# Optimization experiments

Hardware: AMD Instinct MI355X
Metric: run time of the kernel (lower is better)

Reference implementation:

```python
import jax, jax.numpy as jnp
import numpy as np

N = 500000
TOL = 0.01
ALPHA = 0.1
SLOPE = 0.01
EPS = 1e-10


def smooth_relu(x):
    # 0 for x<0; x^2/2 for 0<=x<1; x-1/2 for x>=1 (C1 smooth ReLU)
    return jnp.where(x < 0, 0.0, jnp.where(x < 1, 0.5 * x * x, x - 0.5))


def leaky_relu(x):
    return jnp.where(x >= 0, x, SLOPE * x)


def _xavier(key, shape):
    fan_out, fan_in = shape
    std = np.sqrt(2.0 / (fan_in + fan_out)).astype(np.float32)
    return jax.random.normal(key, shape, dtype=jnp.float32) * std


def setup_inputs() -> dict:
    key = jax.random.key(0)
    ks = jax.random.split(key, 16)
    inp = {
        'X': jax.random.normal(ks[0], (N, 2), dtype=jnp.float32),
        'Xstable': jnp.zeros((N, 2), dtype=jnp.float32),
        'Vl1_w': _xavier(ks[1], (64, 2)),
        'V2x_w': _xavier(ks[2], (64, 2)),
        'V2z_w': _xavier(ks[3], (64, 64)),
        'V3x_w': _xavier(ks[4], (64, 2)),
        'V3z_w': _xavier(ks[5], (64, 64)),
        'Vfx_w': _xavier(ks[6], (1, 2)),
        'Vfz_w': _xavier(ks[7], (1, 64)),
        'f1_w': _xavier(ks[8], (128, 2)),
        'f1_b': jnp.zeros((128,), dtype=jnp.float32),
        'f2_w': _xavier(ks[9], (128, 128)),
        'f2_b': jnp.zeros((128,), dtype=jnp.float32),
        'f3_w': _xavier(ks[10], (128, 128)),
        'f3_b': jnp.zeros((128,), dtype=jnp.float32),
        'f4_w': _xavier(ks[11], (128, 128)),
        'f4_b': jnp.zeros((128,), dtype=jnp.float32),
        'f5_w': _xavier(ks[12], (128, 128)),
        'f5_b': jnp.zeros((128,), dtype=jnp.float32),
        'ff_w': _xavier(ks[13], (2, 128)),
        'ff_b': jnp.zeros((2,), dtype=jnp.float32),
    }
    return inp


def _V_forward(X, Xstable, Vl1_w, V2x_w, V2z_w, V3x_w, V3z_w, Vfx_w, Vfz_w):
    d = X - Xstable                                  # [N,2]
    z1 = smooth_relu(d @ Vl1_w.T)                    # [N,64]
    z2 = smooth_relu(d @ V2x_w.T + z1 @ V2z_w.T)     # [N,64]
    z3 = smooth_relu(d @ V3x_w.T + z2 @ V3z_w.T)     # [N,64]
    zf = smooth_relu(d @ Vfx_w.T + z3 @ Vfz_w.T)     # [N,1]
    vsum = TOL * jnp.sum(d * d, axis=1, keepdims=True)
    return smooth_relu(zf) + vsum                    # [N,1]


def _fhat_forward(X, f1_w, f1_b, f2_w, f2_b, f3_w, f3_b, f4_w, f4_b, f5_w, f5_b, ff_w, ff_b):
    h = leaky_relu(X @ f1_w.T + f1_b)
    h = leaky_relu(h @ f2_w.T + f2_b)
    h = leaky_relu(h @ f3_w.T + f3_b)
    h = leaky_relu(h @ f4_w.T + f4_b)
    h = leaky_relu(h @ f5_w.T + f5_b)
    return h @ ff_w.T + ff_b                         # [N,2]


def reference(X, Xstable, Vl1_w, V2x_w, V2z_w, V3x_w, V3z_w, Vfx_w, Vfz_w,
              f1_w, f1_b, f2_w, f2_b, f3_w, f3_b, f4_w, f4_b, f5_w, f5_b, ff_w, ff_b):
    def Vfn(Xv):
        return _V_forward(Xv, Xstable, Vl1_w, V2x_w, V2z_w, V3x_w, V3z_w, Vfx_w, Vfz_w)

    V, pullback = jax.vjp(Vfn, X)
    gradV = pullback(jnp.ones_like(V))[0]            # dV/dX, [N,2]

    f_hat = _fhat_forward(X, f1_w, f1_b, f2_w, f2_b, f3_w, f3_b,
                          f4_w, f4_b, f5_w, f5_b, ff_w, ff_b)

    Vnorm = jnp.sum(gradV * gradV, axis=1, keepdims=True)      # [N,1]
    fh_V = jnp.sum(f_hat * gradV, axis=1, keepdims=True)       # [N,1]
    f_mul = jax.nn.relu(fh_V + ALPHA * V) / (Vnorm + EPS)      # [N,1]
    f = f_hat - gradV * f_mul                                  # [N,2]
    return f
```

## Files before the change

kernel.cpp:

```cpp
#include <hip/hip_runtime.h>


typedef _Float16 v2h __attribute__((ext_vector_type(2)));
typedef __fp16   v2hf __attribute__((ext_vector_type(2)));
typedef _Float16 v4h __attribute__((ext_vector_type(4)));
typedef _Float16 v8h __attribute__((ext_vector_type(8)));
typedef float    v4f __attribute__((ext_vector_type(4)));

__device__ __forceinline__ v2h cvt_pk(float a, float b){
  v2hf r = __builtin_amdgcn_cvt_pkrtz(a, b);
  union { v2hf f; v2h h; } u; u.f = r;
  return u.h;
}

#define NPTS 500000
#define FUSED_GRID ((NPTS + 255) / 256)

#define BAR_LDS() asm volatile("s_waitcnt lgkmcnt(0)\n\ts_barrier" ::: "memory")

#define OFF_FW    0
#define OFF_V2Z   65536
#define OFF_V3Z   69632
#define OFF_V2ZT  73728
#define OFF_V3ZT  77824
#define OFF_VL1T  81920
#define OFF_V2XT  82048
#define OFF_V3XT  82176
#define OFF_VFZ   82304
#define OFF_FFW   82368
#define OFF_F1W   82624
#define OFF_F1P   82880
#define W16_DATA  86976
#define W16_TOTAL (W16_DATA + 2048)

__device__ __align__(16) _Float16 g_w16[W16_TOTAL];

__device__ __forceinline__ float srelu(float x){
  float c = fminf(fmaxf(x, 0.f), 1.f);
  return c * fmaf(-0.5f, c, x);
}
__device__ __forceinline__ float sreluD(float x){
  return fminf(fmaxf(x, 0.f), 1.f);
}
__device__ __forceinline__ float sreluD_from_z(float z){
  return fminf(sqrtf(2.f * z), 1.f);
}

__device__ __forceinline__ v2h lrelu_pk(float a, float b){
  v2h x = cvt_pk(a, b);
  v2h m = x * (v2h){(_Float16)0.01f, (_Float16)0.01f};
  return __builtin_elementwise_max(x, m);
}
__device__ __forceinline__ v2h srelu_pk(float a, float b){
  v2h x = cvt_pk(a, b);
  const v2h z0 = (v2h){(_Float16)0.f, (_Float16)0.f};
  const v2h o1 = (v2h){(_Float16)1.f, (_Float16)1.f};
  const v2h hf = (v2h){(_Float16)0.5f, (_Float16)0.5f};
  v2h c = __builtin_elementwise_min(__builtin_elementwise_max(x, z0), o1);
  v2h t = x - c * hf;
  return c * t;
}

__global__ __launch_bounds__(256) void prep_kernel(
  const float* __restrict__ f2w, const float* __restrict__ f3w,
  const float* __restrict__ f4w, const float* __restrict__ f5w,
  const float* __restrict__ V2z, const float* __restrict__ V3z,
  const float* __restrict__ Vl1, const float* __restrict__ V2x,
  const float* __restrict__ V3x, const float* __restrict__ Vfz,
  const float* __restrict__ ffw, const float* __restrict__ f1w)
{
  const int i = blockIdx.x * 256 + threadIdx.x;
  if (i >= W16_TOTAL) return;
  if (i >= W16_DATA){ g_w16[i] = (_Float16)0.f; return; }
  float v;
  if (i < 65536){
    const float* W[4] = {f2w, f3w, f4w, f5w};
    v = W[i >> 14][i & 16383];
  } else if (i < 69632)  v = V2z[i - 65536];
  else if (i < 73728)    v = V3z[i - 69632];
  else if (i < 77824){ int r = i - 73728; v = V2z[(r & 63)*64 + (r >> 6)]; }
  else if (i < 81920){ int r = i - 77824; v = V3z[(r & 63)*64 + (r >> 6)]; }
  else if (i < 82048){ int r = i - 81920; v = Vl1[(r & 63)*2 + (r >> 6)]; }
  else if (i < 82176){ int r = i - 82048; v = V2x[(r & 63)*2 + (r >> 6)]; }
  else if (i < 82304){ int r = i - 82176; v = V3x[(r & 63)*2 + (r >> 6)]; }
  else if (i < 82368)    v = Vfz[i - 82304];
  else if (i < 82624)    v = ffw[i - 82368];
  else if (i < 82880)    v = f1w[i - 82624];
  else { int r = i - 82880; int k = r & 31; v = (k < 2) ? f1w[(r >> 5)*2 + k] : 0.f; }
  g_w16[i] = (_Float16)v;
}

__device__ __forceinline__ void fh_layer(_Float16* H,
    const _Float16* __restrict__ Wl, const float* __restrict__ Bp,
    int w, int lm, int q)
{
  const v4f bv = *(const v4f*)(Bp + w*16 + q*4);
  v4f acc[16];
#pragma unroll
  for (int nt = 0; nt < 16; ++nt) acc[nt] = bv;

#pragma unroll
  for (int kt = 0; kt < 4; ++kt){
    const int sw = ((kt*4 + q) ^ lm) << 3;
    v8h A = *(const v8h*)(Wl + (w*16 + lm)*128 + kt*32 + q*8);
#pragma unroll
    for (int nt = 0; nt < 16; ++nt){
      v8h B = *(const v8h*)(H + (nt*16 + lm)*128 + sw);
      acc[nt] = __builtin_amdgcn_mfma_f32_16x16x32_f16(A, B, acc[nt], 0,0,0);
    }
  }
  BAR_LDS();
  const int o0 = w*16 + q*4;
  const int coff = (((o0 >> 3) ^ lm) << 3) + (o0 & 7);
#pragma unroll
  for (int nt = 0; nt < 16; ++nt){
    v4h hv;
    *(v2h*)&hv       = lrelu_pk(acc[nt][0], acc[nt][1]);
    *((v2h*)&hv + 1) = lrelu_pk(acc[nt][2], acc[nt][3]);
    *(v4h*)(H + (nt*16 + lm)*128 + coff) = hv;
  }
  BAR_LDS();
}

__device__ __forceinline__ void vfwd2_l2(_Float16* zoutA, _Float16* zoutB,
    const _Float16* __restrict__ Wz,
    const _Float16* __restrict__ WxT,
    const _Float16* __restrict__ Wl1T,
    float dA0, float dA1, float dB0, float dB1, int lm, int q)
{
  v4f accA[4], accB[4];
#pragma unroll
  for (int mt = 0; mt < 4; ++mt){
    accA[mt] = (v4f){0.f,0.f,0.f,0.f};
    accB[mt] = (v4f){0.f,0.f,0.f,0.f};
  }
  const int rs = lm & 7;
#pragma unroll
  for (int kt = 0; kt < 2; ++kt){
    v8h w0 = *(const v8h*)(Wl1T + kt*32 + q*8);
    v8h w1 = *(const v8h*)(Wl1T + 64 + kt*32 + q*8);
    v8h BA, BB;
#pragma unroll
    for (int j2 = 0; j2 < 4; ++j2){
      const float a0 = (float)w0[2*j2  ], a1 = (float)w0[2*j2+1];
      const float c0 = (float)w1[2*j2  ], c1 = (float)w1[2*j2+1];
      ((v2h*)&BA)[j2] = srelu_pk(fmaf(dA0,a0,dA1*c0), fmaf(dA0,a1,dA1*c1));
      ((v2h*)&BB)[j2] = srelu_pk(fmaf(dB0,a0,dB1*c0), fmaf(dB0,a1,dB1*c1));
    }
#pragma unroll
    for (int mt = 0; mt < 4; ++mt){
      v8h A = *(const v8h*)(Wz + (mt*16 + lm)*64 + kt*32 + q*8);
      accA[mt] = __builtin_amdgcn_mfma_f32_16x16x32_f16(A, BA, accA[mt], 0,0,0);
      accB[mt] = __builtin_amdgcn_mfma_f32_16x16x32_f16(A, BB, accB[mt], 0,0,0);
    }
  }
#pragma unroll
  for (int mt = 0; mt < 4; ++mt){
    const int o0 = mt*16 + q*4;
    const int off = (((o0 >> 3) ^ rs) << 3) + (o0 & 7);
    float vA[4], vB[4];
#pragma unroll
    for (int reg = 0; reg < 4; ++reg){
      const float wx0 = (float)WxT[o0 + reg];
      const float wx1 = (float)WxT[64 + o0 + reg];
      vA[reg] = accA[mt][reg] + wx0*dA0 + wx1*dA1;
      vB[reg] = accB[mt][reg] + wx0*dB0 + wx1*dB1;
    }
    v4h hA, hB;
    *(v2h*)&hA       = srelu_pk(vA[0], vA[1]);
    *((v2h*)&hA + 1) = srelu_pk(vA[2], vA[3]);
    *(v2h*)&hB       = srelu_pk(vB[0], vB[1]);
    *((v2h*)&hB + 1) = srelu_pk(vB[2], vB[3]);
    *(v4h*)(zoutA + lm*64 + off) = hA;
    *(v4h*)(zoutB + lm*64 + off) = hB;
  }
}

__device__ __forceinline__ void vfwd2(const _Float16* zinA, _Float16* zoutA,
    const _Float16* zinB, _Float16* zoutB,
    const _Float16* __restrict__ Wz, const _Float16* __restrict__ WxT,
    float dA0, float dA1, float dB0, float dB1, int lm, int q)
{
  v4f accA[4], accB[4];
#pragma unroll
  for (int mt = 0; mt < 4; ++mt){
    accA[mt] = (v4f){0.f,0.f,0.f,0.f};
    accB[mt] = (v4f){0.f,0.f,0.f,0.f};
  }
  const int rs = lm & 7;
#pragma unroll
  for (int kt = 0; kt < 2; ++kt){
    const int sw = (((kt*4 + q) ^ rs) << 3);
    v8h BA = *(const v8h*)(zinA + lm*64 + sw);
    v8h BB = *(const v8h*)(zinB + lm*64 + sw);
#pragma unroll
    for (int mt = 0; mt < 4; ++mt){
      v8h A = *(const v8h*)(Wz + (mt*16 + lm)*64 + kt*32 + q*8);
      accA[mt] = __builtin_amdgcn_mfma_f32_16x16x32_f16(A, BA, accA[mt], 0,0,0);
      accB[mt] = __builtin_amdgcn_mfma_f32_16x16x32_f16(A, BB, accB[mt], 0,0,0);
    }
  }
#pragma unroll
  for (int mt = 0; mt < 4; ++mt){
    const int o0 = mt*16 + q*4;
    const int off = (((o0 >> 3) ^ rs) << 3) + (o0 & 7);
    float vA[4], vB[4];
#pragma unroll
    for (int reg = 0; reg < 4; ++reg){
      const float wx0 = (float)WxT[o0 + reg];
      const float wx1 = (float)WxT[64 + o0 + reg];
      vA[reg] = accA[mt][reg] + wx0*dA0 + wx1*dA1;
      vB[reg] = accB[mt][reg] + wx0*dB0 + wx1*dB1;
    }
    v4h hA, hB;
    *(v2h*)&hA       = srelu_pk(vA[0], vA[1]);
    *((v2h*)&hA + 1) = srelu_pk(vA[2], vA[3]);
    *(v2h*)&hB       = srelu_pk(vB[0], vB[1]);
    *((v2h*)&hB + 1) = srelu_pk(vB[2], vB[3]);
    *(v4h*)(zoutA + lm*64 + off) = hA;
    *(v4h*)(zoutB + lm*64 + off) = hB;
  }
}

__device__ __forceinline__ void vbwd2(const _Float16* ginA, _Float16* zioA,
    const _Float16* ginB, _Float16* zioB,
    const _Float16* __restrict__ WT, int lm, int q)
{
  v4f accA[4], accB[4];
#pragma unroll
  for (int mt = 0; mt < 4; ++mt){
    accA[mt] = (v4f){0.f,0.f,0.f,0.f};
    accB[mt] = (v4f){0.f,0.f,0.f,0.f};
  }
  const int rs = lm & 7;
#pragma unroll
  for (int kt = 0; kt < 2; ++kt){
    const int sw = (((kt*4 + q) ^ rs) << 3);
    v8h BA = *(const v8h*)(ginA + lm*64 + sw);
    v8h BB = *(const v8h*)(ginB + lm*64 + sw);
#pragma unroll
    for (int mt = 0; mt < 4; ++mt){
      v8h A = *(const v8h*)(WT + (mt*16 + lm)*64 + kt*32 + q*8);
      accA[mt] = __builtin_amdgcn_mfma_f32_16x16x32_f16(A, BA, accA[mt], 0,0,0);
      accB[mt] = __builtin_amdgcn_mfma_f32_16x16x32_f16(A, BB, accB[mt], 0,0,0);
    }
  }
#pragma unroll
  for (int mt = 0; mt < 4; ++mt){
    const int k0 = mt*16 + q*4;
    const int off = (((k0 >> 3) ^ rs) << 3) + (k0 & 7);
    _Float16* pA = zioA + lm*64 + off;
    _Float16* pB = zioB + lm*64 + off;
    v4h zA = *(const v4h*)pA;
    v4h zB = *(const v4h*)pB;
    float sA0 = accA[mt][0] * sreluD_from_z((float)zA[0]);
    float sA1 = accA[mt][1] * sreluD_from_z((float)zA[1]);
    float sA2 = accA[mt][2] * sreluD_from_z((float)zA[2]);
    float sA3 = accA[mt][3] * sreluD_from_z((float)zA[3]);
    float sB0 = accB[mt][0] * sreluD_from_z((float)zB[0]);
    float sB1 = accB[mt][1] * sreluD_from_z((float)zB[1]);
    float sB2 = accB[mt][2] * sreluD_from_z((float)zB[2]);
    float sB3 = accB[mt][3] * sreluD_from_z((float)zB[3]);
    v4h gA, gB;
    *(v2h*)&gA       = cvt_pk(sA0, sA1);
    *((v2h*)&gA + 1) = cvt_pk(sA2, sA3);
    *(v2h*)&gB       = cvt_pk(sB0, sB1);
    *((v2h*)&gB + 1) = cvt_pk(sB2, sB3);
    *(v4h*)pA = gA;
    *(v4h*)pB = gB;
  }
}

__device__ __forceinline__ void vbwd2_l1(_Float16* zioA, _Float16* zioB,
    const _Float16* __restrict__ WT,
    const _Float16* __restrict__ Wl1T,
    float dA0, float dA1, float dB0, float dB1, int lm, int q)
{
  v4f accA[4], accB[4];
#pragma unroll
  for (int mt = 0; mt < 4; ++mt){
    accA[mt] = (v4f){0.f,0.f,0.f,0.f};
    accB[mt] = (v4f){0.f,0.f,0.f,0.f};
  }
  const int rs = lm & 7;
#pragma unroll
  for (int kt = 0; kt < 2; ++kt){
    const int sw = (((kt*4 + q) ^ rs) << 3);
    v8h BA = *(const v8h*)(zioA + lm*64 + sw);
    v8h BB = *(const v8h*)(zioB + lm*64 + sw);
#pragma unroll
    for (int mt = 0; mt < 4; ++mt){
      v8h A = *(const v8h*)(WT + (mt*16 + lm)*64 + kt*32 + q*8);
      accA[mt] = __builtin_amdgcn_mfma_f32_16x16x32_f16(A, BA, accA[mt], 0,0,0);
      accB[mt] = __builtin_amdgcn_mfma_f32_16x16x32_f16(A, BB, accB[mt], 0,0,0);
    }
  }
#pragma unroll
  for (int mt = 0; mt < 4; ++mt){
    const int k0 = mt*16 + q*4;
    const int off = (((k0 >> 3) ^ rs) << 3) + (k0 & 7);
    v4h w0 = *(const v4h*)(Wl1T + k0);
    v4h w1 = *(const v4h*)(Wl1T + 64 + k0);
    float sA[4], sB[4];
#pragma unroll
    for (int reg = 0; reg < 4; ++reg){
      const float a1A = fmaf(dA0, (float)w0[reg], dA1 * (float)w1[reg]);
      const float a1B = fmaf(dB0, (float)w0[reg], dB1 * (float)w1[reg]);
      sA[reg] = accA[mt][reg] * sreluD(a1A);
      sB[reg] = accB[mt][reg] * sreluD(a1B);
    }
    v4h gA, gB;
    *(v2h*)&gA       = cvt_pk(sA[0], sA[1]);
    *((v2h*)&gA + 1) = cvt_pk(sA[2], sA[3]);
    *(v2h*)&gB       = cvt_pk(sB[0], sB[1]);
    *((v2h*)&gB + 1) = cvt_pk(sB[2], sB[3]);
    *(v4h*)(zioA + lm*64 + off) = gA;
    *(v4h*)(zioB + lm*64 + off) = gB;
  }
}

__device__ __forceinline__ void gacc2(v4f& aGA, v4f& aGB,
    const _Float16* __restrict__ WxTbase,
    const _Float16* ZA, const _Float16* ZB, int lm, int q)
{
  const int rs = lm & 7;
#pragma unroll
  for (int kt = 0; kt < 2; ++kt){
    const int sw = (((kt*4 + q) ^ rs) << 3);
    v8h A  = *(const v8h*)(WxTbase + lm*64 + kt*32 + q*8);
    v8h BA = *(const v8h*)(ZA + lm*64 + sw);
    v8h BB = *(const v8h*)(ZB + lm*64 + sw);
    aGA = __builtin_amdgcn_mfma_f32_16x16x32_f16(A, BA, aGA, 0,0,0);
    aGB = __builtin_amdgcn_mfma_f32_16x16x32_f16(A, BB, aGB, 0,0,0);
  }
}

__global__ __launch_bounds__(512, 4) void fused_kernel(
  const float* __restrict__ X, const float* __restrict__ Xst,
  const float* __restrict__ Vfx,
  const float* __restrict__ f1b, const float* __restrict__ f2b,
  const float* __restrict__ f3b, const float* __restrict__ f4b,
  const float* __restrict__ f5b, const float* __restrict__ ffb,
  float* __restrict__ out)
{
  __shared__ __align__(16) char smem[65536];
  _Float16* const H = (_Float16*)smem;

  const int b  = blockIdx.x;
  const int t  = threadIdx.x;
  const int w  = t >> 6;
  const int l  = t & 63;
  const int lm = l & 15;
  const int q  = l >> 4;
  const int rs = lm & 7;
  const int row0 = b*256 + w*32;

  const int r0 = row0 + lm;
  const int r1 = row0 + 16 + lm;
  const int rc0 = r0 < NPTS ? r0 : NPTS-1;
  const int rc1 = r1 < NPTS ? r1 : NPTS-1;
  const float2 x0 = *(const float2*)(X + rc0*2);
  const float2 x1 = *(const float2*)(X + rc1*2);

  {
    v8h Bx0 = (v8h){(_Float16)0.f,(_Float16)0.f,(_Float16)0.f,(_Float16)0.f,
                    (_Float16)0.f,(_Float16)0.f,(_Float16)0.f,(_Float16)0.f};
    v8h Bx1 = Bx0;
    if (q == 0){
      Bx0[0] = (_Float16)x0.x; Bx0[1] = (_Float16)x0.y;
      Bx1[0] = (_Float16)x1.x; Bx1[1] = (_Float16)x1.y;
    }
#pragma unroll
    for (int mt = 0; mt < 8; ++mt){
      const int o0 = mt*16 + q*4;
      const v4f bv = *(const v4f*)(f1b + o0);
      v8h A = *(const v8h*)(g_w16 + OFF_F1P + (mt*16 + lm)*32 + q*8);
      v4f a0 = __builtin_amdgcn_mfma_f32_16x16x32_f16(A, Bx0, bv, 0,0,0);
      v4f a1 = __builtin_amdgcn_mfma_f32_16x16x32_f16(A, Bx1, bv, 0,0,0);
      const int coff = (((o0 >> 3) ^ lm) << 3) + (o0 & 7);
      v4h h0, h1;
      *(v2h*)&h0       = lrelu_pk(a0[0], a0[1]);
      *((v2h*)&h0 + 1) = lrelu_pk(a0[2], a0[3]);
      *(v2h*)&h1       = lrelu_pk(a1[0], a1[1]);
      *((v2h*)&h1 + 1) = lrelu_pk(a1[2], a1[3]);
      *(v4h*)(H + (w*32 + lm)*128 + coff)      = h0;
      *(v4h*)(H + (w*32 + 16 + lm)*128 + coff) = h1;
    }
  }
  BAR_LDS();

  fh_layer(H, g_w16 + OFF_FW,         f2b, w, lm, q);
  fh_layer(H, g_w16 + OFF_FW + 16384, f3b, w, lm, q);
  fh_layer(H, g_w16 + OFF_FW + 32768, f4b, w, lm, q);
  fh_layer(H, g_w16 + OFF_FW + 49152, f5b, w, lm, q);

  float fhA0, fhA1, fhB0, fhB1;
  {
    v4f a0 = (v4f){0.f,0.f,0.f,0.f};
    v4f a1 = (v4f){0.f,0.f,0.f,0.f};
#pragma unroll
    for (int kt = 0; kt < 4; ++kt){
      const int sw = ((kt*4 + q) ^ lm) << 3;
      v8h A  = *(const v8h*)(g_w16 + OFF_FFW + lm*128 + kt*32 + q*8);
      v8h B0 = *(const v8h*)(H + (w*32 + lm)*128 + sw);
      v8h B1 = *(const v8h*)(H + (w*32 + 16 + lm)*128 + sw);
      a0 = __builtin_amdgcn_mfma_f32_16x16x32_f16(A, B0, a0, 0,0,0);
      a1 = __builtin_amdgcn_mfma_f32_16x16x32_f16(A, B1, a1, 0,0,0);
    }
    const float fb0 = ffb[0], fb1 = ffb[1];
    fhA0 = a0[0] + fb0; fhA1 = a0[1] + fb1;
    fhB0 = a1[0] + fb0; fhB1 = a1[1] + fb1;
  }

  _Float16* const ZA2 = (_Float16*)(smem + w*8192);
  _Float16* const ZA3 = ZA2 + 1024;
  _Float16* const ZB2 = ZA2 + 2048;
  _Float16* const ZB3 = ZA2 + 3072;

  const float2 sA = *(const float2*)(Xst + rc0*2);
  const float2 sB = *(const float2*)(Xst + rc1*2);
  const float dA0 = x0.x - sA.x, dA1 = x0.y - sA.y;
  const float dB0 = x1.x - sB.x, dB1 = x1.y - sB.y;
  const float vfx0 = Vfx[0], vfx1 = Vfx[1];

  vfwd2_l2(ZA2, ZB2, g_w16 + OFF_V2Z, g_w16 + OFF_V2XT, g_w16 + OFF_VL1T,
           dA0, dA1, dB0, dB1, lm, q);
  vfwd2(ZA2, ZA3, ZB2, ZB3, g_w16 + OFF_V3Z, g_w16 + OFF_V3XT,
        dA0, dA1, dB0, dB1, lm, q);

  float VVrA, sfA, VVrB, sfB;
  {
    v4f aSA = (v4f){0.f,0.f,0.f,0.f};
    v4f aSB = (v4f){0.f,0.f,0.f,0.f};
#pragma unroll
    for (int kt = 0; kt < 2; ++kt){
      const int sw = (((kt*4 + q) ^ rs) << 3);
      v8h A  = *(const v8h*)(g_w16 + OFF_VFZ + lm*64 + kt*32 + q*8);
      v8h BA = *(const v8h*)(ZA3 + lm*64 + sw);
      v8h BB = *(const v8h*)(ZB3 + lm*64 + sw);
      aSA = __builtin_amdgcn_mfma_f32_16x16x32_f16(A, BA, aSA, 0,0,0);
      aSB = __builtin_amdgcn_mfma_f32_16x16x32_f16(A, BB, aSB, 0,0,0);
    }
    const float afA = fmaf(vfx0, dA0, fmaf(vfx1, dA1, aSA[0]));
    const float zfA = srelu(afA);
    VVrA = srelu(zfA) + 0.01f * fmaf(dA0, dA0, dA1*dA1);
    sfA  = sreluD(zfA) * sreluD(afA);
    const float afB = fmaf(vfx0, dB0, fmaf(vfx1, dB1, aSB[0]));
    const float zfB = srelu(afB);
    VVrB = srelu(zfB) + 0.01f * fmaf(dB0, dB0, dB1*dB1);
    sfB  = sreluD(zfB) * sreluD(afB);
  }

#pragma unroll
  for (int cc = 0; cc < 2; ++cc){
    const int c = q*2 + cc;
    const int sw = ((c ^ rs) << 3);
    v8h vf = *(const v8h*)(g_w16 + OFF_VFZ + c*8);
    _Float16* pA = ZA3 + lm*64 + sw;
    _Float16* pB = ZB3 + lm*64 + sw;
    v8h zA = *(const v8h*)pA;
    v8h zB = *(const v8h*)pB;
    v8h uA, uB;
#pragma unroll
    for (int j2 = 0; j2 < 4; ++j2){
      float a0 = (float)vf[2*j2  ] * sreluD_from_z((float)zA[2*j2  ]);
      float a1 = (float)vf[2*j2+1] * sreluD_from_z((float)zA[2*j2+1]);
      float b0 = (float)vf[2*j2  ] * sreluD_from_z((float)zB[2*j2  ]);
      float b1 = (float)vf[2*j2+1] * sreluD_from_z((float)zB[2*j2+1]);
      ((v2h*)&uA)[j2] = cvt_pk(a0, a1);
      ((v2h*)&uB)[j2] = cvt_pk(b0, b1);
    }
    *(v8h*)pA = uA;
    *(v8h*)pB = uB;
  }

  v4f aGA = (v4f){0.f,0.f,0.f,0.f};
  v4f aGB = (v4f){0.f,0.f,0.f,0.f};

  gacc2(aGA, aGB, g_w16 + OFF_V3XT, ZA3, ZB3, lm, q);
  vbwd2(ZA3, ZA2, ZB3, ZB2, g_w16 + OFF_V3ZT, lm, q);
  gacc2(aGA, aGB, g_w16 + OFF_V2XT, ZA2, ZB2, lm, q);
  vbwd2_l1(ZA2, ZB2, g_w16 + OFF_V2ZT, g_w16 + OFF_VL1T,
           dA0, dA1, dB0, dB1, lm, q);
  gacc2(aGA, aGB, g_w16 + OFF_VL1T, ZA2, ZB2, lm, q);

  const float g0A = fmaf(0.02f, dA0, sfA * (vfx0 + aGA[0]));
  const float g1A = fmaf(0.02f, dA1, sfA * (vfx1 + aGA[1]));
  const float g0B = fmaf(0.02f, dB0, sfB * (vfx0 + aGB[0]));
  const float g1B = fmaf(0.02f, dB1, sfB * (vfx1 + aGB[1]));

  if (q == 0){
    if (r0 < NPTS){
      const float Vn  = fmaf(g0A, g0A, g1A*g1A);
      const float num = fmaf(0.1f, VVrA, fmaf(fhA0, g0A, fhA1*g1A));
      const float fm  = fmaxf(num, 0.f) / (Vn + 1e-10f);
      *(float2*)(out + r0*2) =
        make_float2(fmaf(-g0A, fm, fhA0), fmaf(-g1A, fm, fhA1));
    }
    if (r1 < NPTS){
      const float Vn  = fmaf(g0B, g0B, g1B*g1B);
      const float num = fmaf(0.1f, VVrB, fmaf(fhB0, g0B, fhB1*g1B));
      const float fm  = fmaxf(num, 0.f) / (Vn + 1e-10f);
      *(float2*)(out + r1*2) =
        make_float2(fmaf(-g0B, fm, fhB0), fmaf(-g1B, fm, fhB1));
    }
  }
}

extern "C" void kernel_launch(void* const* d_in, const int* in_sizes, int n_in,
                              void* d_out, int out_size, void* d_ws, size_t ws_size,
                              hipStream_t stream)
{
  (void)d_ws; (void)ws_size; (void)n_in; (void)in_sizes; (void)out_size;
  const float* X   = (const float*)d_in[0];
  const float* Xst = (const float*)d_in[1];
  const float* Vl1 = (const float*)d_in[2];
  const float* V2x = (const float*)d_in[3];
  const float* V2z = (const float*)d_in[4];
  const float* V3x = (const float*)d_in[5];
  const float* V3z = (const float*)d_in[6];
  const float* Vfx = (const float*)d_in[7];
  const float* Vfz = (const float*)d_in[8];
  const float* f1w = (const float*)d_in[9];
  const float* f1b = (const float*)d_in[10];
  const float* f2w = (const float*)d_in[11];
  const float* f2b = (const float*)d_in[12];
  const float* f3w = (const float*)d_in[13];
  const float* f3b = (const float*)d_in[14];
  const float* f4w = (const float*)d_in[15];
  const float* f4b = (const float*)d_in[16];
  const float* f5w = (const float*)d_in[17];
  const float* f5b = (const float*)d_in[18];
  const float* ffw = (const float*)d_in[19];
  const float* ffb = (const float*)d_in[20];

  prep_kernel<<<(W16_TOTAL + 255)/256, 256, 0, stream>>>(
      f2w, f3w, f4w, f5w, V2z, V3z, Vl1, V2x, V3x, Vfz, ffw, f1w);
  fused_kernel<<<FUSED_GRID, 512, 0, stream>>>(
      X, Xst, Vfx, f1b, f2b, f3b, f4b, f5b, ffb, (float*)d_out);
}
```

Measured before the change: 256.2 us.

## Fold d@Wx terms into MFMA and keep layer-2 srelu derivative in registers

Adds zero-padded packed copies of V2x and V3x in the fp16 weight buffer and folds the d·Wx input term into an extra MFMA per output tile, replacing the per-element scalar FMAs and scattered weight loads in the forward V layers. It also keeps the layer-2 smooth-ReLU derivative in 32 registers from the forward pass, so the backward pass no longer reloads z from LDS and recomputes sqrt. The aim is fewer VALU ops and LDS reads, at the cost of more MFMA issues, higher register pressure that may cut occupancy, and rounding d to fp16.

```diff
diff --git a/kernel.cpp b/kernel.cpp
--- a/kernel.cpp
+++ b/kernel.cpp
@@ -30,7 +30,9 @@
 #define OFF_FFW   82368
 #define OFF_F1W   82624
 #define OFF_F1P   82880
-#define W16_DATA  86976
+#define OFF_V2XP  86976
+#define OFF_V3XP  89024
+#define W16_DATA  91072
 #define W16_TOTAL (W16_DATA + 2048)
 
 __device__ __align__(16) _Float16 g_w16[W16_TOTAL];
@@ -86,7 +88,9 @@
   else if (i < 82368)    v = Vfz[i - 82304];
   else if (i < 82624)    v = ffw[i - 82368];
   else if (i < 82880)    v = f1w[i - 82624];
-  else { int r = i - 82880; int k = r & 31; v = (k < 2) ? f1w[(r >> 5)*2 + k] : 0.f; }
+  else if (i < 86976){ int r = i - 82880; int k = r & 31; v = (k < 2) ? f1w[(r >> 5)*2 + k] : 0.f; }
+  else if (i < 89024){ int r = i - 86976; int k = r & 31; v = (k < 2) ? V2x[(r >> 5)*2 + k] : 0.f; }
+  else               { int r = i - 89024; int k = r & 31; v = (k < 2) ? V3x[(r >> 5)*2 + k] : 0.f; }
   g_w16[i] = (_Float16)v;
 }
 
@@ -124,9 +128,12 @@
 
 __device__ __forceinline__ void vfwd2_l2(_Float16* zoutA, _Float16* zoutB,
     const _Float16* __restrict__ Wz,
-    const _Float16* __restrict__ WxT,
+    const _Float16* __restrict__ WxP,
     const _Float16* __restrict__ Wl1T,
-    float dA0, float dA1, float dB0, float dB1, int lm, int q)
+    v8h BdA, v8h BdB,
+    float dA0, float dA1, float dB0, float dB1,
+    float* __restrict__ sdA, float* __restrict__ sdB,
+    int lm, int q)
 {
   v4f accA[4], accB[4];
 #pragma unroll
@@ -135,6 +142,12 @@
     accB[mt] = (v4f){0.f,0.f,0.f,0.f};
   }
   const int rs = lm & 7;
+#pragma unroll
+  for (int mt = 0; mt < 4; ++mt){
+    v8h Ax = *(const v8h*)(WxP + (mt*16 + lm)*32 + q*8);
+    accA[mt] = __builtin_amdgcn_mfma_f32_16x16x32_f16(Ax, BdA, accA[mt], 0,0,0);
+    accB[mt] = __builtin_amdgcn_mfma_f32_16x16x32_f16(Ax, BdB, accB[mt], 0,0,0);
+  }
 #pragma unroll
   for (int kt = 0; kt < 2; ++kt){
     v8h w0 = *(const v8h*)(Wl1T + kt*32 + q*8);
@@ -158,19 +171,16 @@
   for (int mt = 0; mt < 4; ++mt){
     const int o0 = mt*16 + q*4;
     const int off = (((o0 >> 3) ^ rs) << 3) + (o0 & 7);
-    float vA[4], vB[4];
 #pragma unroll
     for (int reg = 0; reg < 4; ++reg){
-      const float wx0 = (float)WxT[o0 + reg];
-      const float wx1 = (float)WxT[64 + o0 + reg];
-      vA[reg] = accA[mt][reg] + wx0*dA0 + wx1*dA1;
-      vB[reg] = accB[mt][reg] + wx0*dB0 + wx1*dB1;
+      sdA[mt*4 + reg] = sreluD(accA[mt][reg]);
+      sdB[mt*4 + reg] = sreluD(accB[mt][reg]);
     }
     v4h hA, hB;
-    *(v2h*)&hA       = srelu_pk(vA[0], vA[1]);
-    *((v2h*)&hA + 1) = srelu_pk(vA[2], vA[3]);
-    *(v2h*)&hB       = srelu_pk(vB[0], vB[1]);
-    *((v2h*)&hB + 1) = srelu_pk(vB[2], vB[3]);
+    *(v2h*)&hA       = srelu_pk(accA[mt][0], accA[mt][1]);
+    *((v2h*)&hA + 1) = srelu_pk(accA[mt][2], accA[mt][3]);
+    *(v2h*)&hB       = srelu_pk(accB[mt][0], accB[mt][1]);
+    *((v2h*)&hB + 1) = srelu_pk(accB[mt][2], accB[mt][3]);
     *(v4h*)(zoutA + lm*64 + off) = hA;
     *(v4h*)(zoutB + lm*64 + off) = hB;
   }
@@ -178,8 +188,9 @@
 
 __device__ __forceinline__ void vfwd2(const _Float16* zinA, _Float16* zoutA,
     const _Float16* zinB, _Float16* zoutB,
-    const _Float16* __restrict__ Wz, const _Float16* __restrict__ WxT,
-    float dA0, float dA1, float dB0, float dB1, int lm, int q)
+    const _Float16* __restrict__ Wz,
+    const _Float16* __restrict__ WxP,
+    v8h BdA, v8h BdB, int lm, int q)
 {
   v4f accA[4], accB[4];
 #pragma unroll
@@ -188,6 +199,12 @@
     accB[mt] = (v4f){0.f,0.f,0.f,0.f};
   }
   const int rs = lm & 7;
+#pragma unroll
+  for (int mt = 0; mt < 4; ++mt){
+    v8h Ax = *(const v8h*)(WxP + (mt*16 + lm)*32 + q*8);
+    accA[mt] = __builtin_amdgcn_mfma_f32_16x16x32_f16(Ax, BdA, accA[mt], 0,0,0);
+    accB[mt] = __builtin_amdgcn_mfma_f32_16x16x32_f16(Ax, BdB, accB[mt], 0,0,0);
+  }
 #pragma unroll
   for (int kt = 0; kt < 2; ++kt){
     const int sw = (((kt*4 + q) ^ rs) << 3);
@@ -204,19 +221,11 @@
   for (int mt = 0; mt < 4; ++mt){
     const int o0 = mt*16 + q*4;
     const int off = (((o0 >> 3) ^ rs) << 3) + (o0 & 7);
-    float vA[4], vB[4];
-#pragma unroll
-    for (int reg = 0; reg < 4; ++reg){
-      const float wx0 = (float)WxT[o0 + reg];
-      const float wx1 = (float)WxT[64 + o0 + reg];
-      vA[reg] = accA[mt][reg] + wx0*dA0 + wx1*dA1;
-      vB[reg] = accB[mt][reg] + wx0*dB0 + wx1*dB1;
-    }
     v4h hA, hB;
-    *(v2h*)&hA       = srelu_pk(vA[0], vA[1]);
-    *((v2h*)&hA + 1) = srelu_pk(vA[2], vA[3]);
-    *(v2h*)&hB       = srelu_pk(vB[0], vB[1]);
-    *((v2h*)&hB + 1) = srelu_pk(vB[2], vB[3]);
+    *(v2h*)&hA       = srelu_pk(accA[mt][0], accA[mt][1]);
+    *((v2h*)&hA + 1) = srelu_pk(accA[mt][2], accA[mt][3]);
+    *(v2h*)&hB       = srelu_pk(accB[mt][0], accB[mt][1]);
+    *((v2h*)&hB + 1) = srelu_pk(accB[mt][2], accB[mt][3]);
     *(v4h*)(zoutA + lm*64 + off) = hA;
     *(v4h*)(zoutB + lm*64 + off) = hB;
   }
@@ -224,7 +233,9 @@
 
 __device__ __forceinline__ void vbwd2(const _Float16* ginA, _Float16* zioA,
     const _Float16* ginB, _Float16* zioB,
-    const _Float16* __restrict__ WT, int lm, int q)
+    const _Float16* __restrict__ WT,
+    const float* __restrict__ sdA, const float* __restrict__ sdB,
+    int lm, int q)
 {
   v4f accA[4], accB[4];
 #pragma unroll
@@ -249,25 +260,13 @@
   for (int mt = 0; mt < 4; ++mt){
     const int k0 = mt*16 + q*4;
     const int off = (((k0 >> 3) ^ rs) << 3) + (k0 & 7);
-    _Float16* pA = zioA + lm*64 + off;
-    _Float16* pB = zioB + lm*64 + off;
-    v4h zA = *(const v4h*)pA;
-    v4h zB = *(const v4h*)pB;
-    float sA0 = accA[mt][0] * sreluD_from_z((float)zA[0]);
-    float sA1 = accA[mt][1] * sreluD_from_z((float)zA[1]);
-    float sA2 = accA[mt][2] * sreluD_from_z((float)zA[2]);
-    float sA3 = accA[mt][3] * sreluD_from_z((float)zA[3]);
-    float sB0 = accB[mt][0] * sreluD_from_z((float)zB[0]);
-    float sB1 = accB[mt][1] * sreluD_from_z((float)zB[1]);
-    float sB2 = accB[mt][2] * sreluD_from_z((float)zB[2]);
-    float sB3 = accB[mt][3] * sreluD_from_z((float)zB[3]);
     v4h gA, gB;
-    *(v2h*)&gA       = cvt_pk(sA0, sA1);
-    *((v2h*)&gA + 1) = cvt_pk(sA2, sA3);
-    *(v2h*)&gB       = cvt_pk(sB0, sB1);
-    *((v2h*)&gB + 1) = cvt_pk(sB2, sB3);
-    *(v4h*)pA = gA;
-    *(v4h*)pB = gB;
+    *(v2h*)&gA       = cvt_pk(accA[mt][0]*sdA[mt*4+0], accA[mt][1]*sdA[mt*4+1]);
+    *((v2h*)&gA + 1) = cvt_pk(accA[mt][2]*sdA[mt*4+2], accA[mt][3]*sdA[mt*4+3]);
+    *(v2h*)&gB       = cvt_pk(accB[mt][0]*sdB[mt*4+0], accB[mt][1]*sdB[mt*4+1]);
+    *((v2h*)&gB + 1) = cvt_pk(accB[mt][2]*sdB[mt*4+2], accB[mt][3]*sdB[mt*4+3]);
+    *(v4h*)(zioA + lm*64 + off) = gA;
+    *(v4h*)(zioB + lm*64 + off) = gB;
   }
 }
 
@@ -423,10 +422,19 @@
   const float dB0 = x1.x - sB.x, dB1 = x1.y - sB.y;
   const float vfx0 = Vfx[0], vfx1 = Vfx[1];
 
-  vfwd2_l2(ZA2, ZB2, g_w16 + OFF_V2Z, g_w16 + OFF_V2XT, g_w16 + OFF_VL1T,
-           dA0, dA1, dB0, dB1, lm, q);
-  vfwd2(ZA2, ZA3, ZB2, ZB3, g_w16 + OFF_V3Z, g_w16 + OFF_V3XT,
-        dA0, dA1, dB0, dB1, lm, q);
+  v8h BdA = (v8h){(_Float16)0.f,(_Float16)0.f,(_Float16)0.f,(_Float16)0.f,
+                  (_Float16)0.f,(_Float16)0.f,(_Float16)0.f,(_Float16)0.f};
+  v8h BdB = BdA;
+  if (q == 0){
+    BdA[0] = (_Float16)dA0; BdA[1] = (_Float16)dA1;
+    BdB[0] = (_Float16)dB0; BdB[1] = (_Float16)dB1;
+  }
+
+  float sdA2[16], sdB2[16];
+  vfwd2_l2(ZA2, ZB2, g_w16 + OFF_V2Z, g_w16 + OFF_V2XP, g_w16 + OFF_VL1T,
+           BdA, BdB, dA0, dA1, dB0, dB1, sdA2, sdB2, lm, q);
+  vfwd2(ZA2, ZA3, ZB2, ZB3, g_w16 + OFF_V3Z, g_w16 + OFF_V3XP,
+        BdA, BdB, lm, q);
 
   float VVrA, sfA, VVrB, sfB;
   {
@@ -478,7 +486,7 @@
   v4f aGB = (v4f){0.f,0.f,0.f,0.f};
 
   gacc2(aGA, aGB, g_w16 + OFF_V3XT, ZA3, ZB3, lm, q);
-  vbwd2(ZA3, ZA2, ZB3, ZB2, g_w16 + OFF_V3ZT, lm, q);
+  vbwd2(ZA3, ZA2, ZB3, ZB2, g_w16 + OFF_V3ZT, sdA2, sdB2, lm, q);
   gacc2(aGA, aGB, g_w16 + OFF_V2XT, ZA2, ZB2, lm, q);
   vbwd2_l1(ZA2, ZB2, g_w16 + OFF_V2ZT, g_w16 + OFF_VL1T,
            dA0, dA1, dB0, dB1, lm, q);
```

New measurement: 254.3 us. Within noise of the previous version (-0.7%).
